# Performance work log

Measured on AMD Instinct MI355X. Metric: run time of the kernel, lower is better.

## Reference

```python
import jax, jax.numpy as jnp
import numpy as np

F_, E_, B_, D_, H_, O_ = 4, 8, 4096, 512, 1024, 512


def setup_inputs() -> dict:
    key = jax.random.key(0)
    ks = jax.random.split(key, 7)
    s = 0.02  # small init scale to keep activations sane
    return {
        "features": jax.random.normal(ks[0], (F_, B_, D_), jnp.float32),
        "W1": jax.random.normal(ks[1], (F_, E_, D_, H_), jnp.float32) * s,
        "b1": jax.random.normal(ks[2], (F_, E_, H_), jnp.float32) * s,
        "W2": jax.random.normal(ks[3], (F_, E_, H_, O_), jnp.float32) * s,
        "b2": jax.random.normal(ks[4], (F_, E_, O_), jnp.float32) * s,
        "Wg": jax.random.normal(ks[5], (F_, D_, E_), jnp.float32) * s,
        "bg": jax.random.normal(ks[6], (F_, E_), jnp.float32) * s,
    }


def reference(features, W1, b1, W2, b2, Wg, bg):
    # Gate: softmax over experts, per feature. [F,B,E]
    gate = jax.nn.softmax(jnp.einsum('fbd,fde->fbe', features, Wg) + bg[:, None, :], axis=-1)
    # All experts computed densely (soft MoE): hidden [F,B,E,H]
    h = jax.nn.relu(jnp.einsum('fbd,fedh->fbeh', features, W1) + b1[:, None, :, :])
    # Expert outputs [F,B,E,O]
    eo = jnp.einsum('fbeh,feho->fbeo', h, W2) + b2[:, None, :, :]
    # Gate-weighted sum over experts, then mean over features -> [B,O]
    weighted = jnp.einsum('fbe,fbeo->fbo', gate, eo)
    return jnp.mean(weighted, axis=0)
```

## Files before the change

### kernel.cpp

```cpp
#include <hip/hip_runtime.h>


#define F_ 4
#define E_ 8
#define B_ 4096
#define D_ 512
#define H_ 1024
#define O_ 512

typedef unsigned short ushort_t;
typedef __bf16 bf16x8 __attribute__((ext_vector_type(8)));
typedef float f32x4 __attribute__((ext_vector_type(4)));
typedef unsigned short ushort8_t __attribute__((ext_vector_type(8)));

__device__ inline ushort_t f2bf(float f) {
  union { float f; unsigned u; } v; v.f = f;
  unsigned r = v.u + 0x7FFFu + ((v.u >> 16) & 1u);
  return (ushort_t)(r >> 16);
}
__device__ inline float bf2f(ushort_t u) {
  union { unsigned u; float f; } v; v.u = ((unsigned)u) << 16;
  return v.f;
}

__device__ inline void async16(const void* g, void* l) {
  __builtin_amdgcn_global_load_lds(
      (const __attribute__((address_space(1))) unsigned int*)g,
      (__attribute__((address_space(3))) unsigned int*)l, 16, 0, 0);
}

__global__ void prep_kernel(const float* __restrict__ features, const float* __restrict__ Wg,
                            const float* __restrict__ bg, float* __restrict__ g2,
                            ushort_t* __restrict__ featbf) {
  const int fb = blockIdx.x;
  const int f = fb >> 12, b = fb & (B_ - 1);
  const int lane = threadIdx.x;
  const float* feat = features + ((size_t)f * B_ + b) * D_;
  const float* wg = Wg + (size_t)f * D_ * E_;
  const int d0 = lane * 8;
  float ff[8];
  *(float4*)&ff[0] = *(const float4*)&feat[d0];
  *(float4*)&ff[4] = *(const float4*)&feat[d0 + 4];
  ushort8_t u;
#pragma unroll
  for (int k = 0; k < 8; ++k) u[k] = f2bf(ff[k]);
  *(ushort8_t*)&featbf[((size_t)f * B_ + b) * D_ + d0] = u;

  float acc[E_] = {0.f, 0.f, 0.f, 0.f, 0.f, 0.f, 0.f, 0.f};
#pragma unroll
  for (int k = 0; k < 8; ++k) {
    const float fv = ff[k];
    const float4 w0 = ((const float4*)(wg + (size_t)(d0 + k) * E_))[0];
    const float4 w1 = ((const float4*)(wg + (size_t)(d0 + k) * E_))[1];
    acc[0] += fv * w0.x; acc[1] += fv * w0.y; acc[2] += fv * w0.z; acc[3] += fv * w0.w;
    acc[4] += fv * w1.x; acc[5] += fv * w1.y; acc[6] += fv * w1.z; acc[7] += fv * w1.w;
  }
#pragma unroll
  for (int off = 32; off >= 1; off >>= 1)
#pragma unroll
    for (int e = 0; e < E_; ++e) acc[e] += __shfl_xor(acc[e], off, 64);
  float lg[E_], mx = -1e30f;
#pragma unroll
  for (int e = 0; e < E_; ++e) { lg[e] = acc[e] + bg[f * E_ + e]; mx = fmaxf(mx, lg[e]); }
  float s = 0.f;
#pragma unroll
  for (int e = 0; e < E_; ++e) { lg[e] = __expf(lg[e] - mx); s += lg[e]; }
  const float inv = 1.f / (s * (float)F_);
  if (lane < E_) g2[((size_t)f * B_ + b) * E_ + lane] = lg[lane] * inv;
}

__global__ void transpose_cast_kernel(const float* __restrict__ in, ushort_t* __restrict__ out,
                                      int R, int C) {
  __shared__ float tile[64][65];
  const size_t zoff = (size_t)blockIdx.z * R * C;
  in += zoff; out += zoff;
  const int tx = threadIdx.x & 63, ty = threadIdx.x >> 6;
  const int r0 = blockIdx.y * 64, c0 = blockIdx.x * 64;
#pragma unroll
  for (int i = 0; i < 16; ++i) {
    const int r = ty + i * 4;
    tile[r][tx] = in[(size_t)(r0 + r) * C + c0 + tx];
  }
  __syncthreads();
#pragma unroll
  for (int i = 0; i < 16; ++i) {
    const int c = ty + i * 4;
    out[(size_t)(c0 + c) * R + r0 + tx] = f2bf(tile[tx][c]);
  }
}


__global__ __launch_bounds__(256, 3) void gemm1_kernel(
    const ushort_t* __restrict__ featbf, const ushort_t* __restrict__ w1t,
    const float* __restrict__ b1, const float* __restrict__ g2,
    ushort_t* __restrict__ Hf, int f0, size_t hfStride) {
  __shared__ __align__(16) ushort_t buf[128 * 136];
  ushort_t* As = buf;
  ushort_t* Bs = buf + 8192;
  const int fy = blockIdx.y, f = f0 + fy;
  const int id = blockIdx.x;
  const int e = id & 7;
  const int s = id >> 3;
  const int n0 = (s & 7) * 128;
  const int m0 = (s >> 3) * 128;
  const ushort_t* A  = featbf + (size_t)f * B_ * D_;
  const ushort_t* Bp = w1t + ((size_t)f * E_ + e) * H_ * D_;
  const float* b1e = b1 + ((size_t)f * E_ + e) * H_;
  const float* g2f = g2 + (size_t)f * B_ * E_;
  ushort_t* HfF = Hf + (size_t)fy * hfStride + (size_t)e * B_ * H_;

  const int t = threadIdx.x, lane = t & 63, w = t >> 6;
  const int wm = w & 1, wn = w >> 1;
  const int lr = lane & 15, q = lane >> 4;

  const int rr = t >> 3;
  const int lc = (t & 7) ^ (rr & 7);
  const char* aSrc = (const char*)A + (size_t)(m0 + rr) * (D_ * 2) + lc * 16;
  const char* bSrc = (const char*)Bp + (size_t)(n0 + rr) * (D_ * 2) + lc * 16;

  f32x4 acc[4][4];
#pragma unroll
  for (int i = 0; i < 4; ++i)
#pragma unroll
    for (int j = 0; j < 4; ++j) acc[i][j] = (f32x4){0.f, 0.f, 0.f, 0.f};

  for (int ks = 0; ks < D_ / 64; ++ks) {
#pragma unroll
    for (int p = 0; p < 4; ++p) {
      async16(aSrc + (size_t)p * (32 * D_ * 2), &As[t * 8 + p * 2048]);
      async16(bSrc + (size_t)p * (32 * D_ * 2), &Bs[t * 8 + p * 2048]);
    }
    aSrc += 128; bSrc += 128;
    __syncthreads();
#pragma unroll
    for (int kh = 0; kh < 2; ++kh) {
      const int ca = (((kh << 2) | q) ^ (lr & 7)) * 8;
      bf16x8 af[4], bfr[4];
#pragma unroll
      for (int i = 0; i < 4; ++i)
        af[i] = *(const bf16x8*)&As[(wm * 64 + i * 16 + lr) * 64 + ca];
#pragma unroll
      for (int j = 0; j < 4; ++j)
        bfr[j] = *(const bf16x8*)&Bs[(wn * 64 + j * 16 + lr) * 64 + ca];
#pragma unroll
      for (int i = 0; i < 4; ++i)
#pragma unroll
        for (int j = 0; j < 4; ++j)
          acc[i][j] = __builtin_amdgcn_mfma_f32_16x16x32_bf16(bfr[j], af[i], acc[i][j], 0, 0, 0);
    }
    __syncthreads();
  }

#pragma unroll
  for (int i = 0; i < 4; ++i) {
    const int ml = wm * 64 + i * 16 + lr;
    const float gv = g2f[(m0 + ml) * E_ + e];
#pragma unroll
    for (int j = 0; j < 4; ++j) {
      const int nl = wn * 64 + j * 16 + q * 4;
      const float4 bb = *(const float4*)&b1e[n0 + nl];
      ushort4 o;
      o.x = f2bf(fmaxf(acc[i][j][0] + bb.x, 0.f) * gv);
      o.y = f2bf(fmaxf(acc[i][j][1] + bb.y, 0.f) * gv);
      o.z = f2bf(fmaxf(acc[i][j][2] + bb.z, 0.f) * gv);
      o.w = f2bf(fmaxf(acc[i][j][3] + bb.w, 0.f) * gv);
      *(ushort4*)&buf[ml * 136 + nl] = o;
    }
  }
  __syncthreads();
  const int row = t >> 1, half = t & 1;
  const ushort_t* src = &buf[row * 136 + half * 64];
  ushort_t* dst = HfF + (size_t)(m0 + row) * H_ + n0 + half * 64;
#pragma unroll
  for (int c = 0; c < 8; ++c)
    *(ushort8_t*)(dst + c * 8) = *(const ushort8_t*)(src + c * 8);
}

__global__ __launch_bounds__(256, 3) void gemm2_kernel(
    const ushort_t* __restrict__ Hf, const ushort_t* __restrict__ w2t,
    const float* __restrict__ b2, const float* __restrict__ g2,
    ushort_t* __restrict__ part, int f0, size_t hfStride) {
  __shared__ __align__(16) ushort_t buf[128 * 136];
  ushort_t* As = buf;
  ushort_t* Bs = buf + 8192;
  const int fy = blockIdx.y, f = f0 + fy;
  const int id = blockIdx.x;
  const int grp = id & 3;
  const int s = id >> 2;
  const int n0 = (s & 3) * 128;
  const int m0 = (s >> 2) * 128;
  const int e0 = grp * 2;
  const float* g2f = g2 + (size_t)f * B_ * E_;

  const int t = threadIdx.x, lane = t & 63, w = t >> 6;
  const int wm = w & 1, wn = w >> 1;
  const int lr = lane & 15, q = lane >> 4;

  const int rr = t >> 3;
  const int lc = (t & 7) ^ (rr & 7);

  f32x4 acc[4][4];
#pragma unroll
  for (int i = 0; i < 4; ++i)
#pragma unroll
    for (int j = 0; j < 4; ++j) acc[i][j] = (f32x4){0.f, 0.f, 0.f, 0.f};

  for (int h = 0; h < 2; ++h) {
    const int e = e0 + h;
    const char* aSrc = (const char*)(Hf + (size_t)fy * hfStride + (size_t)e * B_ * H_) +
                       (size_t)(m0 + rr) * (H_ * 2) + lc * 16;
    const char* bSrc = (const char*)(w2t + ((size_t)f * E_ + e) * O_ * H_) +
                       (size_t)(n0 + rr) * (H_ * 2) + lc * 16;
    for (int ks = 0; ks < H_ / 64; ++ks) {
#pragma unroll
      for (int p = 0; p < 4; ++p) {
        async16(aSrc + (size_t)p * (32 * H_ * 2), &As[t * 8 + p * 2048]);
        async16(bSrc + (size_t)p * (32 * H_ * 2), &Bs[t * 8 + p * 2048]);
      }
      aSrc += 128; bSrc += 128;
      __syncthreads();
#pragma unroll
      for (int kh = 0; kh < 2; ++kh) {
        const int ca = (((kh << 2) | q) ^ (lr & 7)) * 8;
        bf16x8 af[4], bfr[4];
#pragma unroll
        for (int i = 0; i < 4; ++i)
          af[i] = *(const bf16x8*)&As[(wm * 64 + i * 16 + lr) * 64 + ca];
#pragma unroll
        for (int j = 0; j < 4; ++j)
          bfr[j] = *(const bf16x8*)&Bs[(wn * 64 + j * 16 + lr) * 64 + ca];
#pragma unroll
        for (int i = 0; i < 4; ++i)
#pragma unroll
          for (int j = 0; j < 4; ++j)
            acc[i][j] = __builtin_amdgcn_mfma_f32_16x16x32_bf16(bfr[j], af[i], acc[i][j], 0, 0, 0);
      }
      __syncthreads();
    }
  }

  const float* b2e0 = b2 + ((size_t)f * E_ + e0) * O_;
  const float* b2e1 = b2e0 + O_;
#pragma unroll
  for (int i = 0; i < 4; ++i) {
    const int ml = wm * 64 + i * 16 + lr;
    const float gv0 = g2f[(m0 + ml) * E_ + e0];
    const float gv1 = g2f[(m0 + ml) * E_ + e0 + 1];
#pragma unroll
    for (int j = 0; j < 4; ++j) {
      const int nl = wn * 64 + j * 16 + q * 4;
      const int n = n0 + nl;
      const float4 c0 = *(const float4*)&b2e0[n];
      const float4 c1 = *(const float4*)&b2e1[n];
      ushort4 o;
      o.x = f2bf(acc[i][j][0] + gv0 * c0.x + gv1 * c1.x);
      o.y = f2bf(acc[i][j][1] + gv0 * c0.y + gv1 * c1.y);
      o.z = f2bf(acc[i][j][2] + gv0 * c0.z + gv1 * c1.z);
      o.w = f2bf(acc[i][j][3] + gv0 * c0.w + gv1 * c1.w);
      *(ushort4*)&buf[ml * 136 + nl] = o;
    }
  }
  __syncthreads();
  const int row = t >> 1, half = t & 1;
  const ushort_t* src = &buf[row * 136 + half * 64];
  ushort_t* dst = part + (size_t)(f * 4 + grp) * (B_ * O_) + (size_t)(m0 + row) * O_ + n0 + half * 64;
#pragma unroll
  for (int c = 0; c < 8; ++c)
    *(ushort8_t*)(dst + c * 8) = *(const ushort8_t*)(src + c * 8);
}

__global__ void reduce_kernel(const ushort_t* __restrict__ part, float* __restrict__ out) {
  const size_t p = ((size_t)blockIdx.x * 256 + threadIdx.x) * 8;
  float s[8] = {0.f, 0.f, 0.f, 0.f, 0.f, 0.f, 0.f, 0.f};
#pragma unroll
  for (int k = 0; k < F_ * 4; ++k) {
    const ushort8_t u = *(const ushort8_t*)&part[(size_t)k * (B_ * O_) + p];
#pragma unroll
    for (int j = 0; j < 8; ++j) s[j] += bf2f(u[j]);
  }
  float4 o0 = {s[0], s[1], s[2], s[3]}, o1 = {s[4], s[5], s[6], s[7]};
  *(float4*)&out[p] = o0;
  *(float4*)&out[p + 4] = o1;
}

extern "C" void kernel_launch(void* const* d_in, const int* in_sizes, int n_in,
                              void* d_out, int out_size, void* d_ws, size_t ws_size,
                              hipStream_t stream) {
  const float* features = (const float*)d_in[0];
  const float* W1 = (const float*)d_in[1];
  const float* b1 = (const float*)d_in[2];
  const float* W2 = (const float*)d_in[3];
  const float* b2 = (const float*)d_in[4];
  const float* Wg = (const float*)d_in[5];
  const float* bg = (const float*)d_in[6];
  float* out = (float*)d_out;

  char* ws = (char*)d_ws;
  ushort_t* featbf = (ushort_t*)ws;
  ushort_t* w1t    = (ushort_t*)(ws + 16777216);
  ushort_t* w2t    = (ushort_t*)(ws + 50331648);
  float*    g2     = (float*)(ws + 83886080);
  ushort_t* Hf     = (ushort_t*)(ws + 84410368);
  const bool big = ws_size >= (size_t)419954688;
  ushort_t* part   = big ? (ushort_t*)(ws + 352845824)
                         : (ushort_t*)(ws + 151519232);

  prep_kernel<<<F_ * B_, 64, 0, stream>>>(features, Wg, bg, g2, featbf);
  transpose_cast_kernel<<<dim3(H_ / 64, D_ / 64, F_ * E_), 256, 0, stream>>>(W1, w1t, D_, H_);
  transpose_cast_kernel<<<dim3(O_ / 64, H_ / 64, F_ * E_), 256, 0, stream>>>(W2, w2t, H_, O_);

  if (big) {
    gemm1_kernel<<<dim3((B_ / 128) * (H_ / 128) * E_, F_), 256, 0, stream>>>(
        featbf, w1t, b1, g2, Hf, 0, (size_t)E_ * B_ * H_);
    gemm2_kernel<<<dim3((B_ / 128) * (O_ / 128) * 4, F_), 256, 0, stream>>>(
        Hf, w2t, b2, g2, part, 0, (size_t)E_ * B_ * H_);
  } else {
    for (int f = 0; f < F_; ++f) {
      gemm1_kernel<<<dim3((B_ / 128) * (H_ / 128) * E_, 1), 256, 0, stream>>>(
          featbf, w1t, b1, g2, Hf, f, 0);
      gemm2_kernel<<<dim3((B_ / 128) * (O_ / 128) * 4, 1), 256, 0, stream>>>(
          Hf, w2t, b2, g2, part, f, 0);
    }
  }
  reduce_kernel<<<B_ * O_ / 8 / 256, 256, 0, stream>>>(part, out);
}
```

Baseline: 655.3 us.

## Rewrite expert GEMMs with 4-stage async LDS pipeline and larger 512-thread tiles

Both GEMM kernels now use 512-thread blocks with bigger output tiles (256x256 for gemm1, 256x128 for gemm2) and a 4-slot ring of LDS buffers. Global-to-LDS async loads are issued three k-tiles ahead, gated by explicit vmcnt waits and raw s_barrier, and MFMA sections are wrapped in setprio. The goal is to hide global load latency behind MFMA work and cut the per-k-step double syncthreads stalls. gemm2 fuses its two-expert loop into one 64-tile stream. The big-workspace path that launched all features in one grid is dropped, so the kernels always run per-feature, which means more launches and less parallelism per launch.

Result: slower. 668.4 us (+2.0%).

```diff
diff --git a/kernel.cpp b/kernel.cpp
--- a/kernel.cpp
+++ b/kernel.cpp
@@ -27,6 +27,14 @@
   __builtin_amdgcn_global_load_lds(
       (const __attribute__((address_space(1))) unsigned int*)g,
       (__attribute__((address_space(3))) unsigned int*)l, 16, 0, 0);
+}
+
+__device__ inline void barrier_() {
+  __builtin_amdgcn_sched_barrier(0);
+  asm volatile("" ::: "memory");
+  __builtin_amdgcn_s_barrier();
+  asm volatile("" ::: "memory");
+  __builtin_amdgcn_sched_barrier(0);
 }
 
 __global__ void prep_kernel(const float* __restrict__ features, const float* __restrict__ Wg,
@@ -90,114 +98,174 @@
 }
 
 
-__global__ __launch_bounds__(256, 3) void gemm1_kernel(
+#define FSW(r) (((r) + ((r) >> 2)) & 3)
+
+#define G1_VM8 asm volatile("s_waitcnt vmcnt(8)" ::: "memory")
+#define G1_VM4 asm volatile("s_waitcnt vmcnt(4)" ::: "memory")
+#define G1_VM0 asm volatile("s_waitcnt vmcnt(0)" ::: "memory")
+#define G_NOP ((void)0)
+
+#define STAGE1(ktn, p) { \
+    ushort_t* s_ = &lds[((ktn) & 3) * 16384]; \
+    async16(aG + (ktn) * 32 + (p) * (128 * D_), s_ + (p) * 4096 + t * 8); \
+    async16(bG + (ktn) * 32 + (p) * (128 * D_), s_ + 8192 + (p) * 4096 + t * 8); }
+
+#define G1_TILE(kt, STG, VMS) { \
+    const int sl = ((kt) & 3) * 16384; \
+    bf16x8 bfr[4]; \
+    _Pragma("unroll") for (int j = 0; j < 4; ++j) \
+      bfr[j] = *(const bf16x8*)&lds[sl + 8192 + (wn * 64 + j * 16 + lr) * 32 + ca]; \
+    { bf16x8 af[4]; \
+      _Pragma("unroll") for (int i = 0; i < 4; ++i) \
+        af[i] = *(const bf16x8*)&lds[sl + (wm * 128 + i * 16 + lr) * 32 + ca]; \
+      if (STG) { STAGE1((kt) + 3, 0); } \
+      __builtin_amdgcn_s_setprio(1); \
+      _Pragma("unroll") for (int i = 0; i < 4; ++i) \
+        _Pragma("unroll") for (int j = 0; j < 4; ++j) \
+          acc[i][j] = __builtin_amdgcn_mfma_f32_16x16x32_bf16(bfr[j], af[i], acc[i][j], 0, 0, 0); \
+      __builtin_amdgcn_s_setprio(0); \
+      barrier_(); } \
+    { bf16x8 af[4]; \
+      _Pragma("unroll") for (int i = 0; i < 4; ++i) \
+        af[i] = *(const bf16x8*)&lds[sl + (wm * 128 + 64 + i * 16 + lr) * 32 + ca]; \
+      if (STG) { STAGE1((kt) + 3, 1); } \
+      __builtin_amdgcn_s_setprio(1); \
+      _Pragma("unroll") for (int i = 0; i < 4; ++i) \
+        _Pragma("unroll") for (int j = 0; j < 4; ++j) \
+          acc[4 + i][j] = __builtin_amdgcn_mfma_f32_16x16x32_bf16(bfr[j], af[i], acc[4 + i][j], 0, 0, 0); \
+      __builtin_amdgcn_s_setprio(0); \
+      VMS; \
+      barrier_(); } }
+
+__global__ __launch_bounds__(512, 2) void gemm1_kernel(
     const ushort_t* __restrict__ featbf, const ushort_t* __restrict__ w1t,
     const float* __restrict__ b1, const float* __restrict__ g2,
-    ushort_t* __restrict__ Hf, int f0, size_t hfStride) {
-  __shared__ __align__(16) ushort_t buf[128 * 136];
-  ushort_t* As = buf;
-  ushort_t* Bs = buf + 8192;
-  const int fy = blockIdx.y, f = f0 + fy;
+    ushort_t* __restrict__ Hf, int f) {
+  __shared__ __align__(16) ushort_t lds[65536];
   const int id = blockIdx.x;
   const int e = id & 7;
   const int s = id >> 3;
-  const int n0 = (s & 7) * 128;
-  const int m0 = (s >> 3) * 128;
+  const int n0 = (s & 3) * 256;
+  const int m0 = (s >> 2) * 256;
   const ushort_t* A  = featbf + (size_t)f * B_ * D_;
-  const ushort_t* Bp = w1t + ((size_t)f * E_ + e) * H_ * D_;
+  const ushort_t* Bp = w1t + ((size_t)f * E_ + e) * (size_t)H_ * D_;
   const float* b1e = b1 + ((size_t)f * E_ + e) * H_;
   const float* g2f = g2 + (size_t)f * B_ * E_;
-  ushort_t* HfF = Hf + (size_t)fy * hfStride + (size_t)e * B_ * H_;
+  ushort_t* HfE = Hf + (size_t)e * B_ * H_;
 
   const int t = threadIdx.x, lane = t & 63, w = t >> 6;
-  const int wm = w & 1, wn = w >> 1;
+  const int wm = w >> 2, wn = w & 3;
   const int lr = lane & 15, q = lane >> 4;
-
-  const int rr = t >> 3;
-  const int lc = (t & 7) ^ (rr & 7);
-  const char* aSrc = (const char*)A + (size_t)(m0 + rr) * (D_ * 2) + lc * 16;
-  const char* bSrc = (const char*)Bp + (size_t)(n0 + rr) * (D_ * 2) + lc * 16;
-
-  f32x4 acc[4][4];
-#pragma unroll
-  for (int i = 0; i < 4; ++i)
+  const int ca = (q ^ FSW(lr)) * 8;
+
+  const int rr = t >> 2;
+  const int cc = (t & 3) ^ FSW(rr);
+  const ushort_t* aG = A  + (size_t)(m0 + rr) * D_ + cc * 8;
+  const ushort_t* bG = Bp + (size_t)(n0 + rr) * D_ + cc * 8;
+
+  f32x4 acc[8][4];
+#pragma unroll
+  for (int i = 0; i < 8; ++i)
 #pragma unroll
     for (int j = 0; j < 4; ++j) acc[i][j] = (f32x4){0.f, 0.f, 0.f, 0.f};
 
-  for (int ks = 0; ks < D_ / 64; ++ks) {
-#pragma unroll
-    for (int p = 0; p < 4; ++p) {
-      async16(aSrc + (size_t)p * (32 * D_ * 2), &As[t * 8 + p * 2048]);
-      async16(bSrc + (size_t)p * (32 * D_ * 2), &Bs[t * 8 + p * 2048]);
-    }
-    aSrc += 128; bSrc += 128;
-    __syncthreads();
-#pragma unroll
-    for (int kh = 0; kh < 2; ++kh) {
-      const int ca = (((kh << 2) | q) ^ (lr & 7)) * 8;
-      bf16x8 af[4], bfr[4];
-#pragma unroll
-      for (int i = 0; i < 4; ++i)
-        af[i] = *(const bf16x8*)&As[(wm * 64 + i * 16 + lr) * 64 + ca];
-#pragma unroll
-      for (int j = 0; j < 4; ++j)
-        bfr[j] = *(const bf16x8*)&Bs[(wn * 64 + j * 16 + lr) * 64 + ca];
-#pragma unroll
-      for (int i = 0; i < 4; ++i)
-#pragma unroll
-        for (int j = 0; j < 4; ++j)
-          acc[i][j] = __builtin_amdgcn_mfma_f32_16x16x32_bf16(bfr[j], af[i], acc[i][j], 0, 0, 0);
+  STAGE1(0, 0); STAGE1(0, 1);
+  STAGE1(1, 0); STAGE1(1, 1);
+  STAGE1(2, 0); STAGE1(2, 1);
+  G1_VM8;
+  barrier_();
+
+#pragma unroll 4
+  for (int kt = 0; kt < 12; ++kt) G1_TILE(kt, true, G1_VM8);
+  G1_TILE(12, true, G1_VM8);
+  G1_TILE(13, false, G1_VM4);
+  G1_TILE(14, false, G1_VM0);
+  G1_TILE(15, false, G_NOP);
+
+  ushort_t* cb = lds;
+#pragma unroll
+  for (int mh = 0; mh < 2; ++mh) {
+    if (wm == mh) {
+#pragma unroll
+      for (int I = 0; I < 8; ++I) {
+        const int rl = (I >> 2) * 64 + (I & 3) * 16 + lr;
+        const float gv = g2f[(size_t)(m0 + mh * 128 + rl) * E_ + e];
+#pragma unroll
+        for (int j = 0; j < 4; ++j) {
+          const int nl = wn * 64 + j * 16 + q * 4;
+          const float4 bb = *(const float4*)&b1e[n0 + nl];
+          ushort4 o;
+          o.x = f2bf(fmaxf(acc[I][j][0] + bb.x, 0.f) * gv);
+          o.y = f2bf(fmaxf(acc[I][j][1] + bb.y, 0.f) * gv);
+          o.z = f2bf(fmaxf(acc[I][j][2] + bb.z, 0.f) * gv);
+          o.w = f2bf(fmaxf(acc[I][j][3] + bb.w, 0.f) * gv);
+          *(ushort4*)&cb[rl * 264 + nl] = o;
+        }
+      }
     }
     __syncthreads();
-  }
-
-#pragma unroll
-  for (int i = 0; i < 4; ++i) {
-    const int ml = wm * 64 + i * 16 + lr;
-    const float gv = g2f[(m0 + ml) * E_ + e];
-#pragma unroll
-    for (int j = 0; j < 4; ++j) {
-      const int nl = wn * 64 + j * 16 + q * 4;
-      const float4 bb = *(const float4*)&b1e[n0 + nl];
-      ushort4 o;
-      o.x = f2bf(fmaxf(acc[i][j][0] + bb.x, 0.f) * gv);
-      o.y = f2bf(fmaxf(acc[i][j][1] + bb.y, 0.f) * gv);
-      o.z = f2bf(fmaxf(acc[i][j][2] + bb.z, 0.f) * gv);
-      o.w = f2bf(fmaxf(acc[i][j][3] + bb.w, 0.f) * gv);
-      *(ushort4*)&buf[ml * 136 + nl] = o;
-    }
-  }
-  __syncthreads();
-  const int row = t >> 1, half = t & 1;
-  const ushort_t* src = &buf[row * 136 + half * 64];
-  ushort_t* dst = HfF + (size_t)(m0 + row) * H_ + n0 + half * 64;
-#pragma unroll
-  for (int c = 0; c < 8; ++c)
-    *(ushort8_t*)(dst + c * 8) = *(const ushort8_t*)(src + c * 8);
-}
-
-__global__ __launch_bounds__(256, 3) void gemm2_kernel(
+    const int row = t >> 2, seg = t & 3;
+    const ushort_t* src = &cb[row * 264 + seg * 64];
+    ushort_t* dst = HfE + (size_t)(m0 + mh * 128 + row) * H_ + n0 + seg * 64;
+#pragma unroll
+    for (int c = 0; c < 8; ++c)
+      *(ushort8_t*)(dst + c * 8) = *(const ushort8_t*)(src + c * 8);
+    __syncthreads();
+  }
+}
+
+
+#define G2_VM6 asm volatile("s_waitcnt vmcnt(6)" ::: "memory")
+#define G2_VM3 asm volatile("s_waitcnt vmcnt(3)" ::: "memory")
+#define G2_VM0 asm volatile("s_waitcnt vmcnt(0)" ::: "memory")
+
+#define STAGE2(ktn) { \
+    ushort_t* s_ = &lds[((ktn) & 3) * 12288]; \
+    const ushort_t* ag = Hf + (size_t)(e0 + ((ktn) >> 5)) * ((size_t)B_ * H_) + aOff + ((ktn) & 31) * 32; \
+    const ushort_t* bgp = w2tF + (size_t)(e0 + ((ktn) >> 5)) * ((size_t)O_ * H_) + bOff + ((ktn) & 31) * 32; \
+    async16(ag, s_ + t * 8); \
+    async16(ag + 128 * H_, s_ + 4096 + t * 8); \
+    async16(bgp, s_ + 8192 + t * 8); }
+
+#define G2_TILE(kt, STG, VMS) { \
+    const int sl = ((kt) & 3) * 12288; \
+    bf16x8 bfr[4], af[4]; \
+    _Pragma("unroll") for (int j = 0; j < 4; ++j) \
+      bfr[j] = *(const bf16x8*)&lds[sl + 8192 + (wn * 64 + j * 16 + lr) * 32 + ca]; \
+    _Pragma("unroll") for (int i = 0; i < 4; ++i) \
+      af[i] = *(const bf16x8*)&lds[sl + (wm * 64 + i * 16 + lr) * 32 + ca]; \
+    if (STG) { STAGE2((kt) + 3); } \
+    __builtin_amdgcn_s_setprio(1); \
+    _Pragma("unroll") for (int i = 0; i < 4; ++i) \
+      _Pragma("unroll") for (int j = 0; j < 4; ++j) \
+        acc[i][j] = __builtin_amdgcn_mfma_f32_16x16x32_bf16(bfr[j], af[i], acc[i][j], 0, 0, 0); \
+    __builtin_amdgcn_s_setprio(0); \
+    VMS; \
+    barrier_(); }
+
+__global__ __launch_bounds__(512, 2) void gemm2_kernel(
     const ushort_t* __restrict__ Hf, const ushort_t* __restrict__ w2t,
     const float* __restrict__ b2, const float* __restrict__ g2,
-    ushort_t* __restrict__ part, int f0, size_t hfStride) {
-  __shared__ __align__(16) ushort_t buf[128 * 136];
-  ushort_t* As = buf;
-  ushort_t* Bs = buf + 8192;
-  const int fy = blockIdx.y, f = f0 + fy;
+    ushort_t* __restrict__ part, int f) {
+  __shared__ __align__(16) ushort_t lds[49152];
   const int id = blockIdx.x;
   const int grp = id & 3;
   const int s = id >> 2;
   const int n0 = (s & 3) * 128;
-  const int m0 = (s >> 2) * 128;
+  const int m0 = (s >> 2) * 256;
   const int e0 = grp * 2;
+  const ushort_t* w2tF = w2t + (size_t)f * E_ * O_ * H_;
   const float* g2f = g2 + (size_t)f * B_ * E_;
 
   const int t = threadIdx.x, lane = t & 63, w = t >> 6;
-  const int wm = w & 1, wn = w >> 1;
+  const int wm = w >> 1, wn = w & 1;
   const int lr = lane & 15, q = lane >> 4;
-
-  const int rr = t >> 3;
-  const int lc = (t & 7) ^ (rr & 7);
+  const int ca = (q ^ FSW(lr)) * 8;
+
+  const int rr = t >> 2;
+  const int cc = (t & 3) ^ FSW(rr);
+  const size_t aOff = (size_t)(m0 + rr) * H_ + cc * 8;
+  const size_t bOff = (size_t)(n0 + rr) * H_ + cc * 8;
 
   f32x4 acc[4][4];
 #pragma unroll
@@ -205,47 +273,25 @@
 #pragma unroll
     for (int j = 0; j < 4; ++j) acc[i][j] = (f32x4){0.f, 0.f, 0.f, 0.f};
 
-  for (int h = 0; h < 2; ++h) {
-    const int e = e0 + h;
-    const char* aSrc = (const char*)(Hf + (size_t)fy * hfStride + (size_t)e * B_ * H_) +
-                       (size_t)(m0 + rr) * (H_ * 2) + lc * 16;
-    const char* bSrc = (const char*)(w2t + ((size_t)f * E_ + e) * O_ * H_) +
-                       (size_t)(n0 + rr) * (H_ * 2) + lc * 16;
-    for (int ks = 0; ks < H_ / 64; ++ks) {
-#pragma unroll
-      for (int p = 0; p < 4; ++p) {
-        async16(aSrc + (size_t)p * (32 * H_ * 2), &As[t * 8 + p * 2048]);
-        async16(bSrc + (size_t)p * (32 * H_ * 2), &Bs[t * 8 + p * 2048]);
-      }
-      aSrc += 128; bSrc += 128;
-      __syncthreads();
-#pragma unroll
-      for (int kh = 0; kh < 2; ++kh) {
-        const int ca = (((kh << 2) | q) ^ (lr & 7)) * 8;
-        bf16x8 af[4], bfr[4];
-#pragma unroll
-        for (int i = 0; i < 4; ++i)
-          af[i] = *(const bf16x8*)&As[(wm * 64 + i * 16 + lr) * 64 + ca];
-#pragma unroll
-        for (int j = 0; j < 4; ++j)
-          bfr[j] = *(const bf16x8*)&Bs[(wn * 64 + j * 16 + lr) * 64 + ca];
-#pragma unroll
-        for (int i = 0; i < 4; ++i)
-#pragma unroll
-          for (int j = 0; j < 4; ++j)
-            acc[i][j] = __builtin_amdgcn_mfma_f32_16x16x32_bf16(bfr[j], af[i], acc[i][j], 0, 0, 0);
-      }
-      __syncthreads();
-    }
-  }
-
+  STAGE2(0); STAGE2(1); STAGE2(2);
+  G2_VM6;
+  barrier_();
+
+#pragma unroll 4
+  for (int kt = 0; kt < 60; ++kt) G2_TILE(kt, true, G2_VM6);
+  G2_TILE(60, true, G2_VM6);
+  G2_TILE(61, false, G2_VM3);
+  G2_TILE(62, false, G2_VM0);
+  G2_TILE(63, false, G_NOP);
+
+  ushort_t* cb = lds;
   const float* b2e0 = b2 + ((size_t)f * E_ + e0) * O_;
   const float* b2e1 = b2e0 + O_;
 #pragma unroll
   for (int i = 0; i < 4; ++i) {
     const int ml = wm * 64 + i * 16 + lr;
-    const float gv0 = g2f[(m0 + ml) * E_ + e0];
-    const float gv1 = g2f[(m0 + ml) * E_ + e0 + 1];
+    const float gv0 = g2f[(size_t)(m0 + ml) * E_ + e0];
+    const float gv1 = g2f[(size_t)(m0 + ml) * E_ + e0 + 1];
 #pragma unroll
     for (int j = 0; j < 4; ++j) {
       const int nl = wn * 64 + j * 16 + q * 4;
@@ -257,12 +303,12 @@
       o.y = f2bf(acc[i][j][1] + gv0 * c0.y + gv1 * c1.y);
       o.z = f2bf(acc[i][j][2] + gv0 * c0.z + gv1 * c1.z);
       o.w = f2bf(acc[i][j][3] + gv0 * c0.w + gv1 * c1.w);
-      *(ushort4*)&buf[ml * 136 + nl] = o;
+      *(ushort4*)&cb[ml * 136 + nl] = o;
     }
   }
   __syncthreads();
   const int row = t >> 1, half = t & 1;
-  const ushort_t* src = &buf[row * 136 + half * 64];
+  const ushort_t* src = &cb[row * 136 + half * 64];
   ushort_t* dst = part + (size_t)(f * 4 + grp) * (B_ * O_) + (size_t)(m0 + row) * O_ + n0 + half * 64;
 #pragma unroll
   for (int c = 0; c < 8; ++c)
@@ -301,26 +347,15 @@
   ushort_t* w2t    = (ushort_t*)(ws + 50331648);
   float*    g2     = (float*)(ws + 83886080);
   ushort_t* Hf     = (ushort_t*)(ws + 84410368);
-  const bool big = ws_size >= (size_t)419954688;
-  ushort_t* part   = big ? (ushort_t*)(ws + 352845824)
-                         : (ushort_t*)(ws + 151519232);
+  ushort_t* part   = (ushort_t*)(ws + 151519232);
 
   prep_kernel<<<F_ * B_, 64, 0, stream>>>(features, Wg, bg, g2, featbf);
   transpose_cast_kernel<<<dim3(H_ / 64, D_ / 64, F_ * E_), 256, 0, stream>>>(W1, w1t, D_, H_);
   transpose_cast_kernel<<<dim3(O_ / 64, H_ / 64, F_ * E_), 256, 0, stream>>>(W2, w2t, H_, O_);
 
-  if (big) {
-    gemm1_kernel<<<dim3((B_ / 128) * (H_ / 128) * E_, F_), 256, 0, stream>>>(
-        featbf, w1t, b1, g2, Hf, 0, (size_t)E_ * B_ * H_);
-    gemm2_kernel<<<dim3((B_ / 128) * (O_ / 128) * 4, F_), 256, 0, stream>>>(
-        Hf, w2t, b2, g2, part, 0, (size_t)E_ * B_ * H_);
-  } else {
-    for (int f = 0; f < F_; ++f) {
-      gemm1_kernel<<<dim3((B_ / 128) * (H_ / 128) * E_, 1), 256, 0, stream>>>(
-          featbf, w1t, b1, g2, Hf, f, 0);
-      gemm2_kernel<<<dim3((B_ / 128) * (O_ / 128) * 4, 1), 256, 0, stream>>>(
-          Hf, w2t, b2, g2, part, f, 0);
-    }
+  for (int f = 0; f < F_; ++f) {
+    gemm1_kernel<<<512, 512, 0, stream>>>(featbf, w1t, b1, g2, Hf, f);
+    gemm2_kernel<<<256, 512, 0, stream>>>(Hf, w2t, b2, g2, part, f);
   }
   reduce_kernel<<<B_ * O_ / 8 / 256, 256, 0, stream>>>(part, out);
 }
```

## Triple-buffer GEMM K-loops with async LDS prefetch and inline-asm LDS reads

Applied to the files above, without the earlier changes.

Both GEMM kernels now use a 3-slot LDS ring with 32-wide K steps. Global-to-LDS async loads run three stages ahead, gated by explicit vmcnt waits and raw s_barriers, and MFMA sections are wrapped in setprio with ds_read_b128 done through inline asm. The goal is to hide global load latency behind MFMA work instead of syncing twice per K step. The launch path also drops the big-workspace batched variant and always loops over features. This trades one large launch for eight smaller ones and relies on hand-managed waitcnt correctness.

Result: no change. 657.9 us (+0.4%).

```diff
diff --git a/kernel.cpp b/kernel.cpp
--- a/kernel.cpp
+++ b/kernel.cpp
@@ -27,6 +27,15 @@
   __builtin_amdgcn_global_load_lds(
       (const __attribute__((address_space(1))) unsigned int*)g,
       (__attribute__((address_space(3))) unsigned int*)l, 16, 0, 0);
+}
+
+__device__ inline unsigned ldsOff(const void* p) {
+  return (unsigned)(unsigned long long)(const __attribute__((address_space(3))) char*)p;
+}
+__device__ inline bf16x8 dsr128(unsigned byteOff) {
+  bf16x8 r;
+  asm volatile("ds_read_b128 %0, %1" : "=v"(r) : "v"(byteOff));
+  return r;
 }
 
 __global__ void prep_kernel(const float* __restrict__ features, const float* __restrict__ Wg,
@@ -90,33 +99,78 @@
 }
 
 
+#define FSW(r) (((r) + ((r) >> 2)) & 3)
+
+#define VM8 asm volatile("s_waitcnt vmcnt(8)" ::: "memory")
+#define VM4 asm volatile("s_waitcnt vmcnt(4)" ::: "memory")
+#define VM0 asm volatile("s_waitcnt vmcnt(0)" ::: "memory")
+#define VMN ((void)0)
+
+#define G1_STAGE(ktn, SLOT) { \
+    ushort_t* s_ = &lds[(SLOT) * 8192]; \
+    const ushort_t* a_ = aG + (ktn) * 32; \
+    const ushort_t* b_ = bG + (ktn) * 32; \
+    async16(a_,           s_ + t * 8); \
+    async16(a_ + 64 * D_, s_ + 2048 + t * 8); \
+    async16(b_,           s_ + 4096 + t * 8); \
+    async16(b_ + 64 * D_, s_ + 6144 + t * 8); }
+
+#define G2_STAGE(ktn, SLOT) { \
+    ushort_t* s_ = &lds[(SLOT) * 8192]; \
+    const ushort_t* a_ = HfA + (size_t)((ktn) >> 5) * ((size_t)B_ * H_) + aOff + ((ktn) & 31) * 32; \
+    const ushort_t* b_ = w2A + (size_t)((ktn) >> 5) * ((size_t)O_ * H_) + bOff + ((ktn) & 31) * 32; \
+    async16(a_,           s_ + t * 8); \
+    async16(a_ + 64 * H_, s_ + 2048 + t * 8); \
+    async16(b_,           s_ + 4096 + t * 8); \
+    async16(b_ + 64 * H_, s_ + 6144 + t * 8); }
+
+#define GSTEP(kt, SLOT, STG, VMS, STAGEM) { \
+    const unsigned sb = ldsB + (SLOT) * 16384u; \
+    bf16x8 af[4], bfr[4]; \
+    _Pragma("unroll") for (int i_ = 0; i_ < 4; ++i_) af[i_] = dsr128(sb + aRd + i_ * 1024u); \
+    _Pragma("unroll") for (int j_ = 0; j_ < 4; ++j_) bfr[j_] = dsr128(sb + bRd + j_ * 1024u); \
+    asm volatile("s_waitcnt lgkmcnt(0)" ::: "memory"); \
+    __builtin_amdgcn_sched_barrier(0); \
+    __builtin_amdgcn_s_setprio(1); \
+    _Pragma("unroll") for (int i_ = 0; i_ < 4; ++i_) \
+      _Pragma("unroll") for (int j_ = 0; j_ < 4; ++j_) \
+        acc[i_][j_] = __builtin_amdgcn_mfma_f32_16x16x32_bf16(bfr[j_], af[i_], acc[i_][j_], 0, 0, 0); \
+    __builtin_amdgcn_s_setprio(0); \
+    __builtin_amdgcn_sched_barrier(0); \
+    __builtin_amdgcn_s_barrier(); \
+    if (STG) { STAGEM((kt) + 3, SLOT); } \
+    VMS; \
+    __builtin_amdgcn_s_barrier(); \
+    __builtin_amdgcn_sched_barrier(0); }
+
 __global__ __launch_bounds__(256, 3) void gemm1_kernel(
     const ushort_t* __restrict__ featbf, const ushort_t* __restrict__ w1t,
     const float* __restrict__ b1, const float* __restrict__ g2,
-    ushort_t* __restrict__ Hf, int f0, size_t hfStride) {
-  __shared__ __align__(16) ushort_t buf[128 * 136];
-  ushort_t* As = buf;
-  ushort_t* Bs = buf + 8192;
-  const int fy = blockIdx.y, f = f0 + fy;
+    ushort_t* __restrict__ Hf, int f) {
+  __shared__ __align__(16) ushort_t lds[24576];
   const int id = blockIdx.x;
   const int e = id & 7;
   const int s = id >> 3;
   const int n0 = (s & 7) * 128;
   const int m0 = (s >> 3) * 128;
   const ushort_t* A  = featbf + (size_t)f * B_ * D_;
-  const ushort_t* Bp = w1t + ((size_t)f * E_ + e) * H_ * D_;
+  const ushort_t* Bp = w1t + ((size_t)f * E_ + e) * (size_t)H_ * D_;
   const float* b1e = b1 + ((size_t)f * E_ + e) * H_;
   const float* g2f = g2 + (size_t)f * B_ * E_;
-  ushort_t* HfF = Hf + (size_t)fy * hfStride + (size_t)e * B_ * H_;
+  ushort_t* HfE = Hf + (size_t)e * B_ * H_;
 
   const int t = threadIdx.x, lane = t & 63, w = t >> 6;
   const int wm = w & 1, wn = w >> 1;
   const int lr = lane & 15, q = lane >> 4;
-
-  const int rr = t >> 3;
-  const int lc = (t & 7) ^ (rr & 7);
-  const char* aSrc = (const char*)A + (size_t)(m0 + rr) * (D_ * 2) + lc * 16;
-  const char* bSrc = (const char*)Bp + (size_t)(n0 + rr) * (D_ * 2) + lc * 16;
+  const unsigned ldsB = ldsOff(lds);
+  const unsigned caBy = (unsigned)((q ^ FSW(lr)) * 16);
+  const unsigned aRd = (unsigned)((wm * 64 + lr) * 64) + caBy;
+  const unsigned bRd = 8192u + (unsigned)((wn * 64 + lr) * 64) + caBy;
+
+  const int rr = t >> 2;
+  const int cc = (t & 3) ^ FSW(rr);
+  const ushort_t* aG = A  + (size_t)(m0 + rr) * D_ + cc * 8;
+  const ushort_t* bG = Bp + (size_t)(n0 + rr) * D_ + cc * 8;
 
   f32x4 acc[4][4];
 #pragma unroll
@@ -124,37 +178,26 @@
 #pragma unroll
     for (int j = 0; j < 4; ++j) acc[i][j] = (f32x4){0.f, 0.f, 0.f, 0.f};
 
-  for (int ks = 0; ks < D_ / 64; ++ks) {
-#pragma unroll
-    for (int p = 0; p < 4; ++p) {
-      async16(aSrc + (size_t)p * (32 * D_ * 2), &As[t * 8 + p * 2048]);
-      async16(bSrc + (size_t)p * (32 * D_ * 2), &Bs[t * 8 + p * 2048]);
-    }
-    aSrc += 128; bSrc += 128;
-    __syncthreads();
-#pragma unroll
-    for (int kh = 0; kh < 2; ++kh) {
-      const int ca = (((kh << 2) | q) ^ (lr & 7)) * 8;
-      bf16x8 af[4], bfr[4];
-#pragma unroll
-      for (int i = 0; i < 4; ++i)
-        af[i] = *(const bf16x8*)&As[(wm * 64 + i * 16 + lr) * 64 + ca];
-#pragma unroll
-      for (int j = 0; j < 4; ++j)
-        bfr[j] = *(const bf16x8*)&Bs[(wn * 64 + j * 16 + lr) * 64 + ca];
-#pragma unroll
-      for (int i = 0; i < 4; ++i)
-#pragma unroll
-        for (int j = 0; j < 4; ++j)
-          acc[i][j] = __builtin_amdgcn_mfma_f32_16x16x32_bf16(bfr[j], af[i], acc[i][j], 0, 0, 0);
-    }
-    __syncthreads();
-  }
-
+  G1_STAGE(0, 0); G1_STAGE(1, 1); G1_STAGE(2, 2);
+  VM8;
+  __builtin_amdgcn_s_barrier();
+  __builtin_amdgcn_sched_barrier(0);
+
+  for (int b = 0; b < 12; b += 3) {
+    GSTEP(b + 0, 0, 1, VM8, G1_STAGE);
+    GSTEP(b + 1, 1, 1, VM8, G1_STAGE);
+    GSTEP(b + 2, 2, 1, VM8, G1_STAGE);
+  }
+  GSTEP(12, 0, 1, VM8, G1_STAGE);
+  GSTEP(13, 1, 0, VM4, G1_STAGE);
+  GSTEP(14, 2, 0, VM0, G1_STAGE);
+  GSTEP(15, 0, 0, VMN, G1_STAGE);
+
+  ushort_t* cb = lds;
 #pragma unroll
   for (int i = 0; i < 4; ++i) {
     const int ml = wm * 64 + i * 16 + lr;
-    const float gv = g2f[(m0 + ml) * E_ + e];
+    const float gv = g2f[(size_t)(m0 + ml) * E_ + e];
 #pragma unroll
     for (int j = 0; j < 4; ++j) {
       const int nl = wn * 64 + j * 16 + q * 4;
@@ -164,13 +207,13 @@
       o.y = f2bf(fmaxf(acc[i][j][1] + bb.y, 0.f) * gv);
       o.z = f2bf(fmaxf(acc[i][j][2] + bb.z, 0.f) * gv);
       o.w = f2bf(fmaxf(acc[i][j][3] + bb.w, 0.f) * gv);
-      *(ushort4*)&buf[ml * 136 + nl] = o;
+      *(ushort4*)&cb[ml * 136 + nl] = o;
     }
   }
   __syncthreads();
   const int row = t >> 1, half = t & 1;
-  const ushort_t* src = &buf[row * 136 + half * 64];
-  ushort_t* dst = HfF + (size_t)(m0 + row) * H_ + n0 + half * 64;
+  const ushort_t* src = &cb[row * 136 + half * 64];
+  ushort_t* dst = HfE + (size_t)(m0 + row) * H_ + n0 + half * 64;
 #pragma unroll
   for (int c = 0; c < 8; ++c)
     *(ushort8_t*)(dst + c * 8) = *(const ushort8_t*)(src + c * 8);
@@ -179,25 +222,30 @@
 __global__ __launch_bounds__(256, 3) void gemm2_kernel(
     const ushort_t* __restrict__ Hf, const ushort_t* __restrict__ w2t,
     const float* __restrict__ b2, const float* __restrict__ g2,
-    ushort_t* __restrict__ part, int f0, size_t hfStride) {
-  __shared__ __align__(16) ushort_t buf[128 * 136];
-  ushort_t* As = buf;
-  ushort_t* Bs = buf + 8192;
-  const int fy = blockIdx.y, f = f0 + fy;
+    ushort_t* __restrict__ part, int f) {
+  __shared__ __align__(16) ushort_t lds[24576];
   const int id = blockIdx.x;
   const int grp = id & 3;
   const int s = id >> 2;
   const int n0 = (s & 3) * 128;
   const int m0 = (s >> 2) * 128;
   const int e0 = grp * 2;
+  const ushort_t* HfA = Hf + (size_t)e0 * B_ * H_;
+  const ushort_t* w2A = w2t + ((size_t)f * E_ + e0) * (size_t)O_ * H_;
   const float* g2f = g2 + (size_t)f * B_ * E_;
 
   const int t = threadIdx.x, lane = t & 63, w = t >> 6;
   const int wm = w & 1, wn = w >> 1;
   const int lr = lane & 15, q = lane >> 4;
-
-  const int rr = t >> 3;
-  const int lc = (t & 7) ^ (rr & 7);
+  const unsigned ldsB = ldsOff(lds);
+  const unsigned caBy = (unsigned)((q ^ FSW(lr)) * 16);
+  const unsigned aRd = (unsigned)((wm * 64 + lr) * 64) + caBy;
+  const unsigned bRd = 8192u + (unsigned)((wn * 64 + lr) * 64) + caBy;
+
+  const int rr = t >> 2;
+  const int cc = (t & 3) ^ FSW(rr);
+  const size_t aOff = (size_t)(m0 + rr) * H_ + cc * 8;
+  const size_t bOff = (size_t)(n0 + rr) * H_ + cc * 8;
 
   f32x4 acc[4][4];
 #pragma unroll
@@ -205,47 +253,29 @@
 #pragma unroll
     for (int j = 0; j < 4; ++j) acc[i][j] = (f32x4){0.f, 0.f, 0.f, 0.f};
 
-  for (int h = 0; h < 2; ++h) {
-    const int e = e0 + h;
-    const char* aSrc = (const char*)(Hf + (size_t)fy * hfStride + (size_t)e * B_ * H_) +
-                       (size_t)(m0 + rr) * (H_ * 2) + lc * 16;
-    const char* bSrc = (const char*)(w2t + ((size_t)f * E_ + e) * O_ * H_) +
-                       (size_t)(n0 + rr) * (H_ * 2) + lc * 16;
-    for (int ks = 0; ks < H_ / 64; ++ks) {
-#pragma unroll
-      for (int p = 0; p < 4; ++p) {
-        async16(aSrc + (size_t)p * (32 * H_ * 2), &As[t * 8 + p * 2048]);
-        async16(bSrc + (size_t)p * (32 * H_ * 2), &Bs[t * 8 + p * 2048]);
-      }
-      aSrc += 128; bSrc += 128;
-      __syncthreads();
-#pragma unroll
-      for (int kh = 0; kh < 2; ++kh) {
-        const int ca = (((kh << 2) | q) ^ (lr & 7)) * 8;
-        bf16x8 af[4], bfr[4];
-#pragma unroll
-        for (int i = 0; i < 4; ++i)
-          af[i] = *(const bf16x8*)&As[(wm * 64 + i * 16 + lr) * 64 + ca];
-#pragma unroll
-        for (int j = 0; j < 4; ++j)
-          bfr[j] = *(const bf16x8*)&Bs[(wn * 64 + j * 16 + lr) * 64 + ca];
-#pragma unroll
-        for (int i = 0; i < 4; ++i)
-#pragma unroll
-          for (int j = 0; j < 4; ++j)
-            acc[i][j] = __builtin_amdgcn_mfma_f32_16x16x32_bf16(bfr[j], af[i], acc[i][j], 0, 0, 0);
-      }
-      __syncthreads();
-    }
-  }
-
+  G2_STAGE(0, 0); G2_STAGE(1, 1); G2_STAGE(2, 2);
+  VM8;
+  __builtin_amdgcn_s_barrier();
+  __builtin_amdgcn_sched_barrier(0);
+
+  for (int b = 0; b < 60; b += 3) {
+    GSTEP(b + 0, 0, 1, VM8, G2_STAGE);
+    GSTEP(b + 1, 1, 1, VM8, G2_STAGE);
+    GSTEP(b + 2, 2, 1, VM8, G2_STAGE);
+  }
+  GSTEP(60, 0, 1, VM8, G2_STAGE);
+  GSTEP(61, 1, 0, VM4, G2_STAGE);
+  GSTEP(62, 2, 0, VM0, G2_STAGE);
+  GSTEP(63, 0, 0, VMN, G2_STAGE);
+
+  ushort_t* cb = lds;
   const float* b2e0 = b2 + ((size_t)f * E_ + e0) * O_;
   const float* b2e1 = b2e0 + O_;
 #pragma unroll
   for (int i = 0; i < 4; ++i) {
     const int ml = wm * 64 + i * 16 + lr;
-    const float gv0 = g2f[(m0 + ml) * E_ + e0];
-    const float gv1 = g2f[(m0 + ml) * E_ + e0 + 1];
+    const float gv0 = g2f[(size_t)(m0 + ml) * E_ + e0];
+    const float gv1 = g2f[(size_t)(m0 + ml) * E_ + e0 + 1];
 #pragma unroll
     for (int j = 0; j < 4; ++j) {
       const int nl = wn * 64 + j * 16 + q * 4;
@@ -257,12 +287,12 @@
       o.y = f2bf(acc[i][j][1] + gv0 * c0.y + gv1 * c1.y);
       o.z = f2bf(acc[i][j][2] + gv0 * c0.z + gv1 * c1.z);
       o.w = f2bf(acc[i][j][3] + gv0 * c0.w + gv1 * c1.w);
-      *(ushort4*)&buf[ml * 136 + nl] = o;
+      *(ushort4*)&cb[ml * 136 + nl] = o;
     }
   }
   __syncthreads();
   const int row = t >> 1, half = t & 1;
-  const ushort_t* src = &buf[row * 136 + half * 64];
+  const ushort_t* src = &cb[row * 136 + half * 64];
   ushort_t* dst = part + (size_t)(f * 4 + grp) * (B_ * O_) + (size_t)(m0 + row) * O_ + n0 + half * 64;
 #pragma unroll
   for (int c = 0; c < 8; ++c)
@@ -301,26 +331,15 @@
   ushort_t* w2t    = (ushort_t*)(ws + 50331648);
   float*    g2     = (float*)(ws + 83886080);
   ushort_t* Hf     = (ushort_t*)(ws + 84410368);
-  const bool big = ws_size >= (size_t)419954688;
-  ushort_t* part   = big ? (ushort_t*)(ws + 352845824)
-                         : (ushort_t*)(ws + 151519232);
+  ushort_t* part   = (ushort_t*)(ws + 151519232);
 
   prep_kernel<<<F_ * B_, 64, 0, stream>>>(features, Wg, bg, g2, featbf);
   transpose_cast_kernel<<<dim3(H_ / 64, D_ / 64, F_ * E_), 256, 0, stream>>>(W1, w1t, D_, H_);
   transpose_cast_kernel<<<dim3(O_ / 64, H_ / 64, F_ * E_), 256, 0, stream>>>(W2, w2t, H_, O_);
 
-  if (big) {
-    gemm1_kernel<<<dim3((B_ / 128) * (H_ / 128) * E_, F_), 256, 0, stream>>>(
-        featbf, w1t, b1, g2, Hf, 0, (size_t)E_ * B_ * H_);
-    gemm2_kernel<<<dim3((B_ / 128) * (O_ / 128) * 4, F_), 256, 0, stream>>>(
-        Hf, w2t, b2, g2, part, 0, (size_t)E_ * B_ * H_);
-  } else {
-    for (int f = 0; f < F_; ++f) {
-      gemm1_kernel<<<dim3((B_ / 128) * (H_ / 128) * E_, 1), 256, 0, stream>>>(
-          featbf, w1t, b1, g2, Hf, f, 0);
-      gemm2_kernel<<<dim3((B_ / 128) * (O_ / 128) * 4, 1), 256, 0, stream>>>(
-          Hf, w2t, b2, g2, part, f, 0);
-    }
+  for (int f = 0; f < F_; ++f) {
+    gemm1_kernel<<<2048, 256, 0, stream>>>(featbf, w1t, b1, g2, Hf, f);
+    gemm2_kernel<<<512, 256, 0, stream>>>(Hf, w2t, b2, g2, part, f);
   }
   reduce_kernel<<<B_ * O_ / 8 / 256, 256, 0, stream>>>(part, out);
 }
```
